# Performance work log

Hardware: AMD Instinct MI355X
Metric: run time of the kernel (lower is better)

The kernel has to match this reference:

```python
import jax, jax.numpy as jnp
import numpy as np

B, T, H = 32, 2048, 1024


def setup_inputs() -> dict:
    key = jax.random.key(0)
    k1, k2, k3, k4, k5 = jax.random.split(key, 5)
    hidden = jax.random.normal(k1, (1, B, H), dtype=jnp.float32)
    encoder_outputs = jax.random.normal(k2, (B, T, H), dtype=jnp.float32)
    # nn.Linear(2H, H): weight [H, 2H], bias [H]
    lim = 1.0 / np.sqrt(2 * H)
    W = jax.random.uniform(k3, (H, 2 * H), minval=-lim, maxval=lim, dtype=jnp.float32)
    b = jax.random.uniform(k4, (H,), minval=-lim, maxval=lim, dtype=jnp.float32)
    stdv = 1.0 / np.sqrt(H)
    v = jax.random.uniform(k5, (H,), minval=-stdv, maxval=stdv, dtype=jnp.float32)
    return {"hidden": hidden, "encoder_outputs": encoder_outputs, "W": W, "b": b, "v": v}


def reference(hidden, encoder_outputs, W, b, v):
    # hidden: [1, B, H] -> broadcast to [B, T, H]
    h = jnp.broadcast_to(jnp.transpose(hidden, (1, 0, 2)), encoder_outputs.shape)
    x = jnp.concatenate([h, encoder_outputs], axis=2)          # [B, T, 2H]
    energy = jnp.tanh(jnp.einsum('btd,hd->bth', x, W) + b)      # [B, T, H]
    scores = jnp.einsum('h,bth->bt', v, energy)[:, None, :]     # [B, 1, T]
    return jax.nn.softmax(scores, axis=2)
```

## Files before the change

kernel.cpp:

```cpp
#include <hip/hip_runtime.h>
#include <hip/hip_bf16.h>

#define H 1024
#define T 2048
#define B 32
#define BM 128
#define BKC 64
#define NCHUNK 16
#define NCOLT 4
#define BCOLS 256

typedef __attribute__((ext_vector_type(8))) __bf16 bf16x8;
typedef __attribute__((ext_vector_type(16))) float f32x16;
typedef __attribute__((ext_vector_type(8))) unsigned short u16x8;

__device__ __forceinline__ unsigned short f2bf(float f) {
    unsigned int x = __float_as_uint(f);
    x += 0x7fffu + ((x >> 16) & 1u);
    return (unsigned short)(x >> 16);
}

__device__ __forceinline__ float fast_tanh(float x) {
    float t = __expf(2.0f * x);
    return 1.0f - 2.0f * __builtin_amdgcn_rcpf(t + 1.0f);
}

__global__ __launch_bounds__(256) void prep_w_kernel(const float* __restrict__ W,
                                                     unsigned short* __restrict__ Wp) {
    int gid = blockIdx.x * 256 + threadIdx.x;
    int n = gid & (H - 1);
    int kg = gid >> 10;
    const float* srcp = W + (size_t)n * (2 * H) + H + kg * 8;
    float4 f0 = *(const float4*)(srcp);
    float4 f1 = *(const float4*)(srcp + 4);
    u16x8 o;
    o[0] = f2bf(f0.x); o[1] = f2bf(f0.y); o[2] = f2bf(f0.z); o[3] = f2bf(f0.w);
    o[4] = f2bf(f1.x); o[5] = f2bf(f1.y); o[6] = f2bf(f1.z); o[7] = f2bf(f1.w);
    *(u16x8*)(Wp + (size_t)gid * 8) = o;
}

__global__ __launch_bounds__(128) void prep_hp_kernel(const float* __restrict__ hidden,
                                                      const float* __restrict__ W,
                                                      const float* __restrict__ bias,
                                                      float* __restrict__ hp) {
    int b = blockIdx.y;
    int h = blockIdx.x * 128 + threadIdx.x;
    const float* hid = hidden + (size_t)b * H;
    const float* wr = W + (size_t)h * (2 * H);
    float acc = 0.f;
    for (int d = 0; d < H; d += 4) {
        float4 wv = *(const float4*)(wr + d);
        float4 hv = *(const float4*)(hid + d);
        acc += wv.x * hv.x + wv.y * hv.y + wv.z * hv.z + wv.w * hv.w;
    }
    hp[(size_t)b * H + h] = acc + bias[h];
}

#define MFMA32(A, Bv, C) __builtin_amdgcn_mfma_f32_32x32x16_bf16(A, Bv, C, 0, 0, 0)

__global__ __launch_bounds__(512, 4) void energy_kernel(const float* __restrict__ enc,
                                                        const float* __restrict__ hp,
                                                        const float* __restrict__ vvec,
                                                        const unsigned short* __restrict__ Wp,
                                                        float* __restrict__ sc_part) {
    __shared__ __align__(16) unsigned short Abuf[2][BM * BKC];
    __shared__ float scpart[8][BM];

    const int tid = threadIdx.x;
    const int b = blockIdx.z;
    const int t0 = blockIdx.x * BM;
    const int c0 = blockIdx.y * BCOLS;
    const int wave = tid >> 6;
    const int lane = tid & 63;
    const int l31 = lane & 31;
    const int hi = lane >> 5;
    const int wr = wave >> 2;
    const int wc = wave & 3;

    const int st_row = tid >> 2;
    const int st_kq = tid & 3;
    const int ks0 = st_kq * 2, ks1 = ks0 + 1;
    const float* st_src = enc + ((size_t)b * T + t0 + st_row) * H + st_kq * 16;
    char* Ab0 = (char*)&Abuf[0][0];
    char* st_d0 = Ab0 + ks0 * 2048 + (((st_row ^ ks0)) << 4);
    char* st_d1 = Ab0 + ks1 * 2048 + (((st_row ^ ks1)) << 4);

    const unsigned short* wp_base = Wp + (size_t)(c0 + wc * 64 + l31) * 8 + (size_t)hi * (H * 8);

    f32x16 acc00, acc01, acc10, acc11;
#pragma unroll
    for (int i = 0; i < 16; ++i) { acc00[i] = 0.f; acc01[i] = 0.f; acc10[i] = 0.f; acc11[i] = 0.f; }

    const int rv0 = wr * 64 + l31;
    const int rv1 = wr * 64 + 32 + l31;

    {
        float4 f0 = *(const float4*)(st_src);
        float4 f1 = *(const float4*)(st_src + 4);
        float4 f2 = *(const float4*)(st_src + 8);
        float4 f3 = *(const float4*)(st_src + 12);
        u16x8 o0, o1;
        o0[0] = f2bf(f0.x); o0[1] = f2bf(f0.y); o0[2] = f2bf(f0.z); o0[3] = f2bf(f0.w);
        o0[4] = f2bf(f1.x); o0[5] = f2bf(f1.y); o0[6] = f2bf(f1.z); o0[7] = f2bf(f1.w);
        o1[0] = f2bf(f2.x); o1[1] = f2bf(f2.y); o1[2] = f2bf(f2.z); o1[3] = f2bf(f2.w);
        o1[4] = f2bf(f3.x); o1[5] = f2bf(f3.y); o1[6] = f2bf(f3.z); o1[7] = f2bf(f3.w);
        *(u16x8*)st_d0 = o0;
        *(u16x8*)st_d1 = o1;
    }
    bf16x8 bA0 = *(const bf16x8*)(wp_base);
    bf16x8 bA1 = *(const bf16x8*)(wp_base + 256);
    bf16x8 bB0 = *(const bf16x8*)(wp_base + (size_t)1 * (H * 16));
    bf16x8 bB1 = *(const bf16x8*)(wp_base + (size_t)1 * (H * 16) + 256);
    __syncthreads();

#define STEP(KI, C0, C1)                                                       \
    {                                                                          \
        const int kslot = (KI) * 2 + hi;                                       \
        const char* ap = Ab + kslot * 2048;                                    \
        bf16x8 a0 = *(const bf16x8*)(ap + ((rv0 ^ kslot) << 4));               \
        bf16x8 a1 = *(const bf16x8*)(ap + ((rv1 ^ kslot) << 4));               \
        __builtin_amdgcn_s_setprio(1);                                         \
        acc00 = MFMA32(a0, C0, acc00);                                         \
        acc01 = MFMA32(a0, C1, acc01);                                         \
        acc10 = MFMA32(a1, C0, acc10);                                         \
        acc11 = MFMA32(a1, C1, acc11);                                         \
        __builtin_amdgcn_s_setprio(0);                                         \
        const int nit = j * 4 + (KI) + 2;                                      \
        if (nit < 64) {                                                        \
            const unsigned short* bp = wp_base + (size_t)nit * (H * 16);       \
            C0 = *(const bf16x8*)(bp);                                         \
            C1 = *(const bf16x8*)(bp + 256);                                   \
        }                                                                      \
    }

    for (int j = 0; j < NCHUNK; ++j) {
        float4 f0, f1, f2, f3;
        const bool pfA = (j < NCHUNK - 1);
        if (pfA) {
            const float* p = st_src + (j + 1) * BKC;
            f0 = *(const float4*)(p);
            f1 = *(const float4*)(p + 4);
            f2 = *(const float4*)(p + 8);
            f3 = *(const float4*)(p + 12);
        }
        const char* Ab = Ab0 + (j & 1) * 16384;
        STEP(0, bA0, bA1)
        STEP(1, bB0, bB1)
        STEP(2, bA0, bA1)
        STEP(3, bB0, bB1)
        if (pfA) {
            u16x8 o0, o1;
            o0[0] = f2bf(f0.x); o0[1] = f2bf(f0.y); o0[2] = f2bf(f0.z); o0[3] = f2bf(f0.w);
            o0[4] = f2bf(f1.x); o0[5] = f2bf(f1.y); o0[6] = f2bf(f1.z); o0[7] = f2bf(f1.w);
            o1[0] = f2bf(f2.x); o1[1] = f2bf(f2.y); o1[2] = f2bf(f2.z); o1[3] = f2bf(f2.w);
            o1[4] = f2bf(f3.x); o1[5] = f2bf(f3.y); o1[6] = f2bf(f3.z); o1[7] = f2bf(f3.w);
            char* d0 = st_d0 + ((j + 1) & 1) * 16384;
            char* d1 = st_d1 + ((j + 1) & 1) * 16384;
            *(u16x8*)d0 = o0;
            *(u16x8*)d1 = o1;
        }
        __syncthreads();
    }
#undef STEP

    const size_t bH = (size_t)b * H;
    const int col0 = c0 + wc * 64 + l31;
    const int col1 = col0 + 32;
    const float hp0 = hp[bH + col0], hp1 = hp[bH + col1];
    const float v0 = vvec[col0], v1 = vvec[col1];
    float psc[2][16];
#pragma unroll
    for (int r = 0; r < 16; ++r) {
        psc[0][r] = v0 * fast_tanh(acc00[r] + hp0) + v1 * fast_tanh(acc01[r] + hp1);
        psc[1][r] = v0 * fast_tanh(acc10[r] + hp0) + v1 * fast_tanh(acc11[r] + hp1);
    }

#pragma unroll
    for (int rg = 0; rg < 2; ++rg)
#pragma unroll
        for (int r = 0; r < 16; ++r) {
            float s = psc[rg][r];
            s += __shfl_xor(s, 1);
            s += __shfl_xor(s, 2);
            s += __shfl_xor(s, 4);
            s += __shfl_xor(s, 8);
            s += __shfl_xor(s, 16);
            psc[rg][r] = s;
        }
    if (l31 == 0) {
#pragma unroll
        for (int rg = 0; rg < 2; ++rg)
#pragma unroll
            for (int r = 0; r < 16; ++r) {
                int m = wr * 64 + rg * 32 + (r & 3) + 8 * (r >> 2) + 4 * hi;
                scpart[wave][m] = psc[rg][r];
            }
    }
    __syncthreads();
    if (tid < BM) {
        const int wbase = (tid >> 6) * 4;
        float s = scpart[wbase][tid] + scpart[wbase + 1][tid] +
                  scpart[wbase + 2][tid] + scpart[wbase + 3][tid];
        sc_part[((size_t)blockIdx.y * B + b) * T + t0 + tid] = s;
    }
}

__global__ __launch_bounds__(256) void softmax_kernel(const float* __restrict__ sc,
                                                      float* __restrict__ out) {
    int b = blockIdx.x;
    int tid = threadIdx.x;
    int wave = tid >> 6, lane = tid & 63;
    const float* r0 = sc + (size_t)b * T;
    const float* r1 = sc + ((size_t)B + b) * T;
    const float* r2 = sc + ((size_t)2 * B + b) * T;
    const float* r3 = sc + ((size_t)3 * B + b) * T;
    float vals[8];
    float m = -1e30f;
#pragma unroll
    for (int i = 0; i < 8; ++i) {
        int idx = tid + 256 * i;
        vals[i] = (r0[idx] + r1[idx]) + (r2[idx] + r3[idx]);
        m = fmaxf(m, vals[i]);
    }
#pragma unroll
    for (int s = 1; s < 64; s <<= 1) m = fmaxf(m, __shfl_xor(m, s));
    __shared__ float red[4];
    __shared__ float red2[4];
    if (lane == 0) red[wave] = m;
    __syncthreads();
    m = fmaxf(fmaxf(red[0], red[1]), fmaxf(red[2], red[3]));
    float sum = 0.f;
#pragma unroll
    for (int i = 0; i < 8; ++i) { vals[i] = expf(vals[i] - m); sum += vals[i]; }
#pragma unroll
    for (int s = 1; s < 64; s <<= 1) sum += __shfl_xor(sum, s);
    if (lane == 0) red2[wave] = sum;
    __syncthreads();
    sum = red2[0] + red2[1] + red2[2] + red2[3];
    float inv = 1.0f / sum;
#pragma unroll
    for (int i = 0; i < 8; ++i) out[(size_t)b * T + tid + 256 * i] = vals[i] * inv;
}

extern "C" void kernel_launch(void* const* d_in, const int* in_sizes, int n_in,
                              void* d_out, int out_size, void* d_ws, size_t ws_size,
                              hipStream_t stream) {
    (void)in_sizes; (void)n_in; (void)out_size; (void)ws_size;
    const float* hidden = (const float*)d_in[0];
    const float* enc    = (const float*)d_in[1];
    const float* W      = (const float*)d_in[2];
    const float* bias   = (const float*)d_in[3];
    const float* v      = (const float*)d_in[4];
    float* out = (float*)d_out;

    unsigned short* Wp = (unsigned short*)d_ws;
    float* hp = (float*)((char*)d_ws + 2 * 1024 * 1024);
    float* sc = (float*)((char*)d_ws + 2 * 1024 * 1024 + 128 * 1024);

    prep_w_kernel<<<dim3(512), dim3(256), 0, stream>>>(W, Wp);
    prep_hp_kernel<<<dim3(8, B), dim3(128), 0, stream>>>(hidden, W, bias, hp);
    energy_kernel<<<dim3(T / BM, NCOLT, B), dim3(512), 0, stream>>>(enc, hp, v, Wp, sc);
    softmax_kernel<<<dim3(B), dim3(256), 0, stream>>>(sc, out);
}
```

Baseline: 258.6 us.

## Pre-convert encoder outputs to bf16 MFMA-ready layout and load A from global directly

Adds a separate prep kernel that converts the fp32 encoder outputs into a tiled bf16 layout matching the MFMA operand order. The energy kernel then loads A fragments straight from global memory into registers, with the same register prefetch used for W, and drops the LDS double buffer and per-chunk barriers. The aim is to remove LDS traffic, synchronisation and the conversion that each of the four column-tile blocks repeated. In exchange it adds a full extra pass over the 256MB input (read fp32, write 128MB bf16, then read that bf16 four times), which can cost more than it saves on a memory-bound kernel.

```diff
diff --git a/kernel.cpp b/kernel.cpp
--- a/kernel.cpp
+++ b/kernel.cpp
@@ -5,8 +5,6 @@
 #define T 2048
 #define B 32
 #define BM 128
-#define BKC 64
-#define NCHUNK 16
 #define NCOLT 4
 #define BCOLS 256
 
@@ -37,6 +35,22 @@
     o[0] = f2bf(f0.x); o[1] = f2bf(f0.y); o[2] = f2bf(f0.z); o[3] = f2bf(f0.w);
     o[4] = f2bf(f1.x); o[5] = f2bf(f1.y); o[6] = f2bf(f1.z); o[7] = f2bf(f1.w);
     *(u16x8*)(Wp + (size_t)gid * 8) = o;
+}
+
+__global__ __launch_bounds__(256) void prep_enc_kernel(const float* __restrict__ enc,
+                                                       unsigned short* __restrict__ Ap) {
+    int gid = blockIdx.x * 256 + threadIdx.x;
+    int row = gid & 127;
+    int kg = (gid >> 7) & 127;
+    int bt = gid >> 14;
+    int b = bt >> 4, tile = bt & 15;
+    const float* src = enc + ((size_t)b * T + tile * 128 + row) * H + kg * 8;
+    float4 f0 = *(const float4*)(src);
+    float4 f1 = *(const float4*)(src + 4);
+    u16x8 o;
+    o[0] = f2bf(f0.x); o[1] = f2bf(f0.y); o[2] = f2bf(f0.z); o[3] = f2bf(f0.w);
+    o[4] = f2bf(f1.x); o[5] = f2bf(f1.y); o[6] = f2bf(f1.z); o[7] = f2bf(f1.w);
+    *(u16x8*)(Ap + (size_t)gid * 8) = o;
 }
 
 __global__ __launch_bounds__(128) void prep_hp_kernel(const float* __restrict__ hidden,
@@ -58,12 +72,11 @@
 
 #define MFMA32(A, Bv, C) __builtin_amdgcn_mfma_f32_32x32x16_bf16(A, Bv, C, 0, 0, 0)
 
-__global__ __launch_bounds__(512, 4) void energy_kernel(const float* __restrict__ enc,
+__global__ __launch_bounds__(512, 4) void energy_kernel(const unsigned short* __restrict__ Ap,
                                                         const float* __restrict__ hp,
                                                         const float* __restrict__ vvec,
                                                         const unsigned short* __restrict__ Wp,
                                                         float* __restrict__ sc_part) {
-    __shared__ __align__(16) unsigned short Abuf[2][BM * BKC];
     __shared__ float scpart[8][BM];
 
     const int tid = threadIdx.x;
@@ -77,89 +90,47 @@
     const int wr = wave >> 2;
     const int wc = wave & 3;
 
-    const int st_row = tid >> 2;
-    const int st_kq = tid & 3;
-    const int ks0 = st_kq * 2, ks1 = ks0 + 1;
-    const float* st_src = enc + ((size_t)b * T + t0 + st_row) * H + st_kq * 16;
-    char* Ab0 = (char*)&Abuf[0][0];
-    char* st_d0 = Ab0 + ks0 * 2048 + (((st_row ^ ks0)) << 4);
-    char* st_d1 = Ab0 + ks1 * 2048 + (((st_row ^ ks1)) << 4);
-
+    const int bt = b * 16 + blockIdx.x;
+    const unsigned short* ap0 = Ap + ((size_t)bt * 128 + hi) * 1024 + (size_t)(wr * 64 + l31) * 8;
+    const unsigned short* ap1 = ap0 + 32 * 8;
     const unsigned short* wp_base = Wp + (size_t)(c0 + wc * 64 + l31) * 8 + (size_t)hi * (H * 8);
 
     f32x16 acc00, acc01, acc10, acc11;
 #pragma unroll
     for (int i = 0; i < 16; ++i) { acc00[i] = 0.f; acc01[i] = 0.f; acc10[i] = 0.f; acc11[i] = 0.f; }
 
-    const int rv0 = wr * 64 + l31;
-    const int rv1 = wr * 64 + 32 + l31;
-
-    {
-        float4 f0 = *(const float4*)(st_src);
-        float4 f1 = *(const float4*)(st_src + 4);
-        float4 f2 = *(const float4*)(st_src + 8);
-        float4 f3 = *(const float4*)(st_src + 12);
-        u16x8 o0, o1;
-        o0[0] = f2bf(f0.x); o0[1] = f2bf(f0.y); o0[2] = f2bf(f0.z); o0[3] = f2bf(f0.w);
-        o0[4] = f2bf(f1.x); o0[5] = f2bf(f1.y); o0[6] = f2bf(f1.z); o0[7] = f2bf(f1.w);
-        o1[0] = f2bf(f2.x); o1[1] = f2bf(f2.y); o1[2] = f2bf(f2.z); o1[3] = f2bf(f2.w);
-        o1[4] = f2bf(f3.x); o1[5] = f2bf(f3.y); o1[6] = f2bf(f3.z); o1[7] = f2bf(f3.w);
-        *(u16x8*)st_d0 = o0;
-        *(u16x8*)st_d1 = o1;
-    }
+    bf16x8 aA0 = *(const bf16x8*)(ap0);
+    bf16x8 aA1 = *(const bf16x8*)(ap1);
     bf16x8 bA0 = *(const bf16x8*)(wp_base);
     bf16x8 bA1 = *(const bf16x8*)(wp_base + 256);
-    bf16x8 bB0 = *(const bf16x8*)(wp_base + (size_t)1 * (H * 16));
-    bf16x8 bB1 = *(const bf16x8*)(wp_base + (size_t)1 * (H * 16) + 256);
-    __syncthreads();
-
-#define STEP(KI, C0, C1)                                                       \
+    bf16x8 aB0 = *(const bf16x8*)(ap0 + 2048);
+    bf16x8 aB1 = *(const bf16x8*)(ap1 + 2048);
+    bf16x8 bB0 = *(const bf16x8*)(wp_base + (size_t)H * 16);
+    bf16x8 bB1 = *(const bf16x8*)(wp_base + (size_t)H * 16 + 256);
+
+#define STEP(KI, AC0, AC1, BC0, BC1)                                           \
     {                                                                          \
-        const int kslot = (KI) * 2 + hi;                                       \
-        const char* ap = Ab + kslot * 2048;                                    \
-        bf16x8 a0 = *(const bf16x8*)(ap + ((rv0 ^ kslot) << 4));               \
-        bf16x8 a1 = *(const bf16x8*)(ap + ((rv1 ^ kslot) << 4));               \
         __builtin_amdgcn_s_setprio(1);                                         \
-        acc00 = MFMA32(a0, C0, acc00);                                         \
-        acc01 = MFMA32(a0, C1, acc01);                                         \
-        acc10 = MFMA32(a1, C0, acc10);                                         \
-        acc11 = MFMA32(a1, C1, acc11);                                         \
+        acc00 = MFMA32(AC0, BC0, acc00);                                       \
+        acc01 = MFMA32(AC0, BC1, acc01);                                       \
+        acc10 = MFMA32(AC1, BC0, acc10);                                       \
+        acc11 = MFMA32(AC1, BC1, acc11);                                       \
         __builtin_amdgcn_s_setprio(0);                                         \
         const int nit = j * 4 + (KI) + 2;                                      \
         if (nit < 64) {                                                        \
+            AC0 = *(const bf16x8*)(ap0 + (size_t)nit * 2048);                  \
+            AC1 = *(const bf16x8*)(ap1 + (size_t)nit * 2048);                  \
             const unsigned short* bp = wp_base + (size_t)nit * (H * 16);       \
-            C0 = *(const bf16x8*)(bp);                                         \
-            C1 = *(const bf16x8*)(bp + 256);                                   \
+            BC0 = *(const bf16x8*)(bp);                                        \
+            BC1 = *(const bf16x8*)(bp + 256);                                  \
         }                                                                      \
     }
 
-    for (int j = 0; j < NCHUNK; ++j) {
-        float4 f0, f1, f2, f3;
-        const bool pfA = (j < NCHUNK - 1);
-        if (pfA) {
-            const float* p = st_src + (j + 1) * BKC;
-            f0 = *(const float4*)(p);
-            f1 = *(const float4*)(p + 4);
-            f2 = *(const float4*)(p + 8);
-            f3 = *(const float4*)(p + 12);
-        }
-        const char* Ab = Ab0 + (j & 1) * 16384;
-        STEP(0, bA0, bA1)
-        STEP(1, bB0, bB1)
-        STEP(2, bA0, bA1)
-        STEP(3, bB0, bB1)
-        if (pfA) {
-            u16x8 o0, o1;
-            o0[0] = f2bf(f0.x); o0[1] = f2bf(f0.y); o0[2] = f2bf(f0.z); o0[3] = f2bf(f0.w);
-            o0[4] = f2bf(f1.x); o0[5] = f2bf(f1.y); o0[6] = f2bf(f1.z); o0[7] = f2bf(f1.w);
-            o1[0] = f2bf(f2.x); o1[1] = f2bf(f2.y); o1[2] = f2bf(f2.z); o1[3] = f2bf(f2.w);
-            o1[4] = f2bf(f3.x); o1[5] = f2bf(f3.y); o1[6] = f2bf(f3.z); o1[7] = f2bf(f3.w);
-            char* d0 = st_d0 + ((j + 1) & 1) * 16384;
-            char* d1 = st_d1 + ((j + 1) & 1) * 16384;
-            *(u16x8*)d0 = o0;
-            *(u16x8*)d1 = o1;
-        }
-        __syncthreads();
+    for (int j = 0; j < 16; ++j) {
+        STEP(0, aA0, aA1, bA0, bA1)
+        STEP(1, aB0, aB1, bB0, bB1)
+        STEP(2, aA0, aA1, bA0, bA1)
+        STEP(3, aB0, aB1, bB0, bB1)
     }
 #undef STEP
 
@@ -256,9 +227,11 @@
     unsigned short* Wp = (unsigned short*)d_ws;
     float* hp = (float*)((char*)d_ws + 2 * 1024 * 1024);
     float* sc = (float*)((char*)d_ws + 2 * 1024 * 1024 + 128 * 1024);
+    unsigned short* Ap = (unsigned short*)((char*)d_ws + 4 * 1024 * 1024);
 
     prep_w_kernel<<<dim3(512), dim3(256), 0, stream>>>(W, Wp);
     prep_hp_kernel<<<dim3(8, B), dim3(128), 0, stream>>>(hidden, W, bias, hp);
-    energy_kernel<<<dim3(T / BM, NCOLT, B), dim3(512), 0, stream>>>(enc, hp, v, Wp, sc);
+    prep_enc_kernel<<<dim3(32768), dim3(256), 0, stream>>>(enc, Ap);
+    energy_kernel<<<dim3(T / BM, NCOLT, B), dim3(512), 0, stream>>>(Ap, hp, v, Wp, sc);
     softmax_kernel<<<dim3(B), dim3(256), 0, stream>>>(sc, out);
 }
```

Result: slower. 344.1 us (+33.1%).
